# Optimization experiments

Measured on AMD Instinct MI355X. Metric: run time of the kernel, lower is better.

The kernel has to match this reference:

```python
import jax, jax.numpy as jnp
import numpy as np

DIM = 1024      # main_dim
HEADS = 16      # attn_num
HEAD = DIM // HEADS
S = 1024        # seq len per half
BH = 1          # batch per half (x_input batch = 2*BH)
PE = 16; FE = 16      # experts per group
PD = 512; FD = 512    # expert hidden dims
DS = 2048             # shared_expert_dim
K = 4                 # top_k routed experts
EPS = 1e-5
THETA = 10000.0
SCALE_P = 1.0; SCALE_F = 1.0


def rmsnorm(x, w, eps=EPS):
    return x * jax.lax.rsqrt(jnp.mean(x * x, -1, keepdims=True) + eps) * w


def rope(x, theta=THETA):
    # x: [b, h, s, a]; matches RotaryEmb: y1 = x1*cos + x2*sin, y2 = -x1*sin + x2*cos
    a = x.shape[-1]; s = x.shape[2]
    inv = (1.0 / theta) ** (jnp.arange(0, a, 2, dtype=jnp.float32) / a)
    fr = jnp.arange(s, dtype=jnp.float32)[:, None] * inv[None, :]   # [s, a//2]
    cos, sin = jnp.cos(fr), jnp.sin(fr)
    x1, x2 = jnp.split(x, 2, -1)
    return jnp.concatenate([x1 * cos + x2 * sin, -x1 * sin + x2 * cos], -1)


def moe(xt, block, idx, sc):
    # xt: [T, d]; block: [3, E, d, f] (gate/up/down SwiGLU); idx, sc: [T, K]
    g = jnp.einsum('td,edf->tef', xt, block[0])
    u = jnp.einsum('td,edf->tef', xt, block[1])
    h = jax.nn.silu(g) * u
    out_all = jnp.einsum('tef,edf->ted', h, block[2])        # per-expert outputs
    sel = jnp.take_along_axis(out_all, idx[:, :, None], 1)   # [T, K, d]
    return jnp.sum(sel * sc[:, :, None], 1)


def setup_inputs():
    key = jax.random.key(0)
    ks = jax.random.split(key, 16)
    w = 0.02  # param scale for numerical sanity
    d = {}
    d['x_input'] = jax.random.normal(ks[0], (2 * BH, S, DIM), jnp.float32)
    d['p_indices'] = jax.random.randint(ks[1], (BH * S, K), 0, PE)
    d['p_values'] = jax.random.normal(ks[2], (BH * S, K), jnp.float32)
    d['f_indices'] = jax.random.randint(ks[3], (BH * S, K), 0, FE)
    d['f_values'] = jax.random.normal(ks[4], (BH * S, K), jnp.float32)
    d['attn_norm_w'] = jnp.ones((DIM,), jnp.float32)
    d['ffn_norm_w'] = jnp.ones((DIM,), jnp.float32)
    d['W_attn'] = jax.random.normal(ks[5], (DIM, 3 * DIM), jnp.float32) * w
    d['W_attn_o'] = jax.random.normal(ks[6], (DIM, DIM), jnp.float32) * w
    d['ffn_up_w'] = jax.random.normal(ks[7], (DIM, 2 * DS), jnp.float32) * w
    d['ffn_down_w'] = jax.random.normal(ks[8], (DS, DIM), jnp.float32) * w
    d['p_ffn_experts'] = jax.random.normal(ks[9], (3, PE, DIM, PD), jnp.float32) * w
    d['f_ffn_experts'] = jax.random.normal(ks[10], (3, FE, DIM, FD), jnp.float32) * w
    d['p_token_keys'] = jax.random.normal(ks[11], (DIM, PE), jnp.float32) * w
    d['f_token_keys'] = jax.random.normal(ks[12], (DIM, FE), jnp.float32) * w
    d['p_router_bias'] = jnp.zeros((PE,), jnp.float32)
    d['f_router_bias'] = jnp.zeros((FE,), jnp.float32)
    return d


def reference(x_input, p_indices, p_values, f_indices, f_values,
              attn_norm_w, ffn_norm_w, W_attn, W_attn_o, ffn_up_w, ffn_down_w,
              p_ffn_experts, f_ffn_experts, p_token_keys, f_token_keys,
              p_router_bias, f_router_bias):
    B2, s, dim = x_input.shape
    b = B2 // 2
    # attention block
    x = rmsnorm(x_input, attn_norm_w)
    xq, xk, xv = jnp.split(x @ W_attn, 3, -1)
    heads = lambda t: t.reshape(B2, s, HEADS, HEAD).transpose(0, 2, 1, 3)
    xq, xk, xv = heads(xq), heads(xk), heads(xv)
    xq, xk = rope(xq), rope(xk)
    # dual interleave: '(c b) h s a -> b h (s c) a', c=2
    il = lambda t: t.reshape(2, b, HEADS, s, HEAD).transpose(1, 2, 3, 0, 4).reshape(b, HEADS, 2 * s, HEAD)
    q, k, v = il(xq), il(xk), il(xv)
    scores = jnp.einsum('bhqa,bhka->bhqk', q, k) / jnp.sqrt(jnp.float32(HEAD))
    causal = jnp.tril(jnp.ones((2 * s, 2 * s), bool))
    attn = jax.nn.softmax(jnp.where(causal, scores, -jnp.inf), -1)
    o = jnp.einsum('bhqk,bhka->bhqa', attn, v)
    # de-interleave: 'b h (s c) a -> (c b) s (h a)'
    o = o.reshape(b, HEADS, s, 2, HEAD).transpose(3, 0, 2, 1, 4).reshape(B2, s, dim)
    x_ffn_input = o @ W_attn_o + x_input
    x_ffn = rmsnorm(x_ffn_input, ffn_norm_w)
    p_x = x_ffn[:b].reshape(-1, dim)
    f_x = x_ffn[b:].reshape(-1, dim)
    # router: token keys + bias, sigmoid, normalize
    p_vals = p_values + jnp.take_along_axis(p_x @ p_token_keys, p_indices, -1) + p_router_bias[p_indices]
    f_vals = f_values + jnp.take_along_axis(f_x @ f_token_keys, f_indices, -1) + f_router_bias[f_indices]
    p_sc = jax.nn.sigmoid(p_vals)
    p_sc = p_sc / jnp.sum(p_sc, -1, keepdims=True) * SCALE_P
    f_sc = jax.nn.sigmoid(f_vals)
    f_sc = f_sc / jnp.sum(f_sc, -1, keepdims=True) * SCALE_F
    py = moe(p_x, p_ffn_experts, p_indices, p_sc).reshape(b, s, dim)
    fy = moe(f_x, f_ffn_experts, f_indices, f_sc).reshape(b, s, dim)
    y = jnp.concatenate([py, fy], 0) + x_ffn_input
    # shared expert (SwiGLU)
    x1, x2 = jnp.split(x_ffn @ ffn_up_w, 2, -1)
    y = y + (jax.nn.silu(x1) * x2) @ ffn_down_w
    return y
```

## Files before the change

### kernel.cpp

```cpp
#include <hip/hip_runtime.h>


#define T_TOT   2048
#define DMODEL  1024
#define NHEADS  16
#define NEXP    16
#define FDIM    512
#define DSH     2048
#define NPAIR   8192

typedef __attribute__((ext_vector_type(4))) float          f32x4;
typedef __attribute__((ext_vector_type(8))) short          s16x8;
typedef __attribute__((ext_vector_type(8))) unsigned short u16x8;
typedef __attribute__((ext_vector_type(2))) unsigned int   u32x2;

__device__ __forceinline__ float sigm(float x) { return 1.0f / (1.0f + __expf(-x)); }

__device__ __forceinline__ unsigned short bf16r(float f) {
    union { float f; unsigned int u; } v; v.f = f;
    unsigned int r = v.u + 0x7fffu + ((v.u >> 16) & 1u);
    return (unsigned short)(r >> 16);
}

__device__ __forceinline__ unsigned int cvtpk(float lo, float hi) {
    unsigned int r;
    asm("v_cvt_pk_bf16_f32 %0, %1, %2" : "=v"(r) : "v"(lo), "v"(hi));
    return r;
}

__device__ __forceinline__ float ubf(unsigned short u) {
    union { unsigned int i; float f; } v; v.i = (unsigned int)u << 16; return v.f;
}

__device__ __forceinline__ int pair2tok(int p) {
    return ((p >> 12) << 10) + ((p & 4095) >> 2);
}

__global__ void rmsnorm_kernel(const float* __restrict__ x,
                               const float* __restrict__ w,
                               unsigned short* __restrict__ out) {
    int t = blockIdx.x, tid = threadIdx.x;
    float4 xv = *(const float4*)(x + (size_t)t * DMODEL + tid * 4);
    __shared__ float rb[256];
    rb[tid] = xv.x*xv.x + xv.y*xv.y + xv.z*xv.z + xv.w*xv.w;
    __syncthreads();
    for (int s = 128; s > 0; s >>= 1) { if (tid < s) rb[tid] += rb[tid+s]; __syncthreads(); }
    float scale = rsqrtf(rb[0] * (1.0f/1024.0f) + 1e-5f);
    float4 wv = *(const float4*)(w + tid * 4);
    u32x2 pv;
    pv.x = cvtpk(xv.x * scale * wv.x, xv.y * scale * wv.y);
    pv.y = cvtpk(xv.z * scale * wv.z, xv.w * scale * wv.w);
    *(u32x2*)(out + (size_t)t * DMODEL + tid * 4) = pv;
}

__global__ void rope_kernel(unsigned short* __restrict__ qkv) {
    int t = blockIdx.x, tid = threadIdx.x;
    int s = t & 1023;
    unsigned short* row = qkv + (size_t)t * 3072;
    for (int pp = tid; pp < 512; pp += 256) {
        int h = pp >> 5, i = pp & 31;
        float fr = (float)s * exp2f(-0.41524101186092028f * (float)i);
        float sn, cs;
        sincosf(fr, &sn, &cs);
        int o1 = (h << 6) + i, o2 = o1 + 32;
        float x1 = ubf(row[o1]), x2 = ubf(row[o2]);
        row[o1] = bf16r(x1 * cs + x2 * sn);
        row[o2] = bf16r(x2 * cs - x1 * sn);
        x1 = ubf(row[1024 + o1]); x2 = ubf(row[1024 + o2]);
        row[1024 + o1] = bf16r(x1 * cs + x2 * sn);
        row[1024 + o2] = bf16r(x2 * cs - x1 * sn);
    }
}

__global__ __launch_bounds__(256) void attn_mfma_kernel(
        const unsigned short* __restrict__ qkv,
        unsigned short* __restrict__ attn_out) {
    int qt = blockIdx.x, h = blockIdx.y;
    __shared__ alignas(16) unsigned short Qs[64][72];
    __shared__ alignas(16) unsigned short Ks[64][72];
    __shared__ alignas(16) unsigned short Vt[64][72];
    __shared__ alignas(16) unsigned short Ps[4][16][72];
    int tid = threadIdx.x;
    int w = tid >> 6, lane = tid & 63;
    int lr = lane & 15, lkg = lane >> 4, lk = lkg << 3;
    int kr = tid >> 3, kc = (tid & 7) << 3;

    #pragma unroll
    for (int i = 0; i < 2; ++i) {
        int rr = kr + 32 * i;
        int p = qt * 64 + rr;
        int t = ((p & 1) << 10) + (p >> 1);
        u16x8 q = *(const u16x8*)(qkv + (size_t)t * 3072 + (h << 6) + kc);
        unsigned int* dst = (unsigned int*)&Qs[rr][kc];
        dst[0] = cvtpk(ubf(q[0]) * 0.125f, ubf(q[1]) * 0.125f);
        dst[1] = cvtpk(ubf(q[2]) * 0.125f, ubf(q[3]) * 0.125f);
        dst[2] = cvtpk(ubf(q[4]) * 0.125f, ubf(q[5]) * 0.125f);
        dst[3] = cvtpk(ubf(q[6]) * 0.125f, ubf(q[7]) * 0.125f);
    }
    u16x8 pkv[2], pvv[2];
    #pragma unroll
    for (int i = 0; i < 2; ++i) {
        int rr = kr + 32 * i;
        int t = ((rr & 1) << 10) + (rr >> 1);
        const unsigned short* b = qkv + (size_t)t * 3072 + (h << 6) + kc;
        pkv[i] = *(const u16x8*)(b + 1024);
        pvv[i] = *(const u16x8*)(b + 2048);
    }
    __syncthreads();
    s16x8 qa0 = *(const s16x8*)&Qs[(w << 4) + lr][lk];
    s16x8 qa1 = *(const s16x8*)&Qs[(w << 4) + lr][32 + lk];

    float m[4], l[4];
    f32x4 oacc[4];
    #pragma unroll
    for (int r = 0; r < 4; ++r) { m[r] = -1e30f; l[r] = 0.0f; }
    #pragma unroll
    for (int df = 0; df < 4; ++df) oacc[df] = (f32x4)0.0f;

    int qrow_base = qt * 64 + w * 16 + lkg * 4;

    for (int kb = 0; kb <= qt; ++kb) {
        __syncthreads();
        u16x8 ck[2], cv[2];
        #pragma unroll
        for (int i = 0; i < 2; ++i) { ck[i] = pkv[i]; cv[i] = pvv[i]; }
        if (kb + 1 <= qt) {
            #pragma unroll
            for (int i = 0; i < 2; ++i) {
                int rr = kr + 32 * i;
                int p = (kb + 1) * 64 + rr;
                int t = ((p & 1) << 10) + (p >> 1);
                const unsigned short* b = qkv + (size_t)t * 3072 + (h << 6) + kc;
                pkv[i] = *(const u16x8*)(b + 1024);
                pvv[i] = *(const u16x8*)(b + 2048);
            }
        }
        #pragma unroll
        for (int i = 0; i < 2; ++i) {
            int rr = kr + 32 * i;
            *(u16x8*)&Ks[rr][kc] = ck[i];
            #pragma unroll
            for (int j = 0; j < 8; ++j) {
                int vrow = kc + j;
                int sw = ((vrow >> 3) & 7) << 3;
                Vt[vrow][rr ^ sw] = cv[i][j];
            }
        }
        __syncthreads();

        f32x4 s[4];
        #pragma unroll
        for (int nf = 0; nf < 4; ++nf) {
            s16x8 b0 = *(const s16x8*)&Ks[nf * 16 + lr][lk];
            s16x8 b1 = *(const s16x8*)&Ks[nf * 16 + lr][32 + lk];
            f32x4 z = (f32x4)0.0f;
            z = __builtin_amdgcn_mfma_f32_16x16x32_bf16(qa0, b0, z, 0, 0, 0);
            z = __builtin_amdgcn_mfma_f32_16x16x32_bf16(qa1, b1, z, 0, 0, 0);
            s[nf] = z;
        }
        if (kb == qt) {
            #pragma unroll
            for (int nf = 0; nf < 4; ++nf) {
                int kcol = kb * 64 + nf * 16 + lr;
                #pragma unroll
                for (int r = 0; r < 4; ++r)
                    if (kcol > qrow_base + r) s[nf][r] = -1e30f;
            }
        }
        float mloc[4];
        #pragma unroll
        for (int r = 0; r < 4; ++r)
            mloc[r] = fmaxf(fmaxf(s[0][r], s[1][r]), fmaxf(s[2][r], s[3][r]));
        #pragma unroll
        for (int r = 0; r < 4; ++r) {
            mloc[r] = fmaxf(mloc[r], __shfl_xor(mloc[r], 1));
            mloc[r] = fmaxf(mloc[r], __shfl_xor(mloc[r], 2));
            mloc[r] = fmaxf(mloc[r], __shfl_xor(mloc[r], 4));
            mloc[r] = fmaxf(mloc[r], __shfl_xor(mloc[r], 8));
        }
        float alpha[4], psum[4];
        #pragma unroll
        for (int r = 0; r < 4; ++r) {
            float mnew = fmaxf(m[r], mloc[r]);
            alpha[r] = __expf(m[r] - mnew);
            m[r] = mnew;
            psum[r] = 0.0f;
        }
        #pragma unroll
        for (int nf = 0; nf < 4; ++nf)
            #pragma unroll
            for (int r = 0; r < 4; ++r) {
                float pv2 = __expf(s[nf][r] - m[r]);
                s[nf][r] = pv2;
                psum[r] += pv2;
            }
        #pragma unroll
        for (int r = 0; r < 4; ++r) {
            psum[r] += __shfl_xor(psum[r], 1);
            psum[r] += __shfl_xor(psum[r], 2);
            psum[r] += __shfl_xor(psum[r], 4);
            psum[r] += __shfl_xor(psum[r], 8);
            l[r] = l[r] * alpha[r] + psum[r];
        }
        #pragma unroll
        for (int nf = 0; nf < 4; ++nf)
            #pragma unroll
            for (int r = 0; r < 4; ++r)
                Ps[w][lkg * 4 + r][nf * 16 + lr] = bf16r(s[nf][r]);
        #pragma unroll
        for (int df = 0; df < 4; ++df)
            #pragma unroll
            for (int r = 0; r < 4; ++r)
                oacc[df][r] *= alpha[r];
        s16x8 pa0 = *(const s16x8*)&Ps[w][lr][lk];
        s16x8 pa1 = *(const s16x8*)&Ps[w][lr][32 + lk];
        #pragma unroll
        for (int df = 0; df < 4; ++df) {
            int vr = df * 16 + lr;
            int sw = ((vr >> 3) & 7) << 3;
            s16x8 v0 = *(const s16x8*)&Vt[vr][lk ^ sw];
            s16x8 v1 = *(const s16x8*)&Vt[vr][(32 + lk) ^ sw];
            oacc[df] = __builtin_amdgcn_mfma_f32_16x16x32_bf16(pa0, v0, oacc[df], 0, 0, 0);
            oacc[df] = __builtin_amdgcn_mfma_f32_16x16x32_bf16(pa1, v1, oacc[df], 0, 0, 0);
        }
    }

    float invl[4];
    #pragma unroll
    for (int r = 0; r < 4; ++r) invl[r] = 1.0f / l[r];
    #pragma unroll
    for (int r = 0; r < 4; ++r) {
        int qrow = qrow_base + r;
        int t = ((qrow & 1) << 10) + (qrow >> 1);
        unsigned short* op = attn_out + (size_t)t * 1024 + (h << 6) + lr;
        #pragma unroll
        for (int df = 0; df < 4; ++df)
            op[df * 16] = bf16r(oacc[df][r] * invl[r]);
    }
}

__global__ void router_kernel(const unsigned short* __restrict__ xffn,
        const float* __restrict__ p_keys, const float* __restrict__ f_keys,
        const int* __restrict__ p_idx, const int* __restrict__ f_idx,
        const float* __restrict__ p_val, const float* __restrict__ f_val,
        const float* __restrict__ p_bias, const float* __restrict__ f_bias,
        float* __restrict__ sc) {
    int tl = blockIdx.x, hf = blockIdx.y;
    int t = hf * 1024 + tl;
    const float* keys = hf ? f_keys : p_keys;
    const int* idx    = hf ? f_idx  : p_idx;
    const float* val  = hf ? f_val  : p_val;
    const float* bias = hf ? f_bias : p_bias;
    int tid = threadIdx.x;
    float acc[16];
    #pragma unroll
    for (int e = 0; e < 16; ++e) acc[e] = 0.0f;
    const unsigned short* x = xffn + (size_t)t * DMODEL;
    for (int d = tid; d < 1024; d += 256) {
        float xd = ubf(x[d]);
        const float* kr = keys + d * 16;
        #pragma unroll
        for (int e4 = 0; e4 < 4; ++e4) {
            float4 kv = *(const float4*)(kr + e4 * 4);
            acc[e4*4+0] += xd * kv.x;
            acc[e4*4+1] += xd * kv.y;
            acc[e4*4+2] += xd * kv.z;
            acc[e4*4+3] += xd * kv.w;
        }
    }
    #pragma unroll
    for (int e = 0; e < 16; ++e) {
        float v = acc[e];
        v += __shfl_down(v, 32); v += __shfl_down(v, 16); v += __shfl_down(v, 8);
        v += __shfl_down(v, 4);  v += __shfl_down(v, 2);  v += __shfl_down(v, 1);
        acc[e] = v;
    }
    __shared__ float part[4][16];
    __shared__ float logit[16];
    __shared__ float sg[4];
    int wave = tid >> 6, ln = tid & 63;
    if (ln == 0) {
        #pragma unroll
        for (int e = 0; e < 16; ++e) part[wave][e] = acc[e];
    }
    __syncthreads();
    if (tid < 16) logit[tid] = part[0][tid] + part[1][tid] + part[2][tid] + part[3][tid];
    __syncthreads();
    if (tid < 4) {
        int ii = idx[tl * 4 + tid];
        float v = val[tl * 4 + tid] + logit[ii] + bias[ii];
        sg[tid] = 1.0f / (1.0f + expf(-v));
    }
    __syncthreads();
    if (tid < 4) {
        float ssum = sg[0] + sg[1] + sg[2] + sg[3];
        sc[t * 4 + tid] = sg[tid] / ssum;
    }
}

__global__ __launch_bounds__(1024) void buckets_kernel(
        const int* __restrict__ p_idx, const int* __restrict__ f_idx,
        int* __restrict__ counts, int* __restrict__ offsets,
        int* __restrict__ pair_p) {
    __shared__ int lcnt[32], loff[32], lcur[32];
    int tid = threadIdx.x;
    if (tid < 32) { lcnt[tid] = 0; lcur[tid] = 0; }
    __syncthreads();
    for (int p = tid; p < NPAIR; p += 1024) {
        int hf = p >> 12, rem = p & 4095;
        int e = (hf ? f_idx : p_idx)[rem];
        atomicAdd(&lcnt[(hf << 4) + e], 1);
    }
    __syncthreads();
    if (tid == 0) {
        int o = 0;
        for (int b = 0; b < 32; ++b) { loff[b] = o; o += lcnt[b]; }
    }
    __syncthreads();
    for (int p = tid; p < NPAIR; p += 1024) {
        int hf = p >> 12, rem = p & 4095;
        int e = (hf ? f_idx : p_idx)[rem];
        int b = (hf << 4) + e;
        int pos = atomicAdd(&lcur[b], 1);
        pair_p[loff[b] + pos] = p;
    }
    if (tid < 32) { counts[tid] = lcnt[tid]; offsets[tid] = loff[tid]; }
}

template<int MODE, int BN2, int OUTBF>
__global__ __launch_bounds__(256) void mfma_gemm(
        const unsigned short* __restrict__ A, const float* __restrict__ B,
        void* __restrict__ Cv, const float* __restrict__ resid,
        int M, int N, int K) {
    constexpr int NI = BN2 / 32;
    __shared__ alignas(16) unsigned short As[128][40];
    __shared__ alignas(16) unsigned short Bs[BN2][40];
    int tid = threadIdx.x;
    int m0 = blockIdx.y * 128, n0 = blockIdx.x * BN2;
    int w = tid >> 6, lane = tid & 63;
    int wm = (w >> 1) * 64, wn = (w & 1) * (BN2 / 2);
    int lr = lane & 15, lk = (lane >> 4) << 3;
    int ar = tid >> 2, ac = (tid & 3) << 3;
    int bn = (tid >> 3) << 2, bk = (tid & 7) << 2;
    bool bact = true;
    if (BN2 == 64) bact = (tid < 128);
    const unsigned short* Ap0 = A + (size_t)(m0 + ar) * K + ac;
    const unsigned short* Ap1 = Ap0 + (size_t)64 * K;
    const float* Bp = B + (size_t)bk * N + n0 + bn;

    f32x4 acc[4][NI] = {};
    u16x8 a0c, a1c, a0n, a1n;
    f32x4 b_c[4], b_n[4];
    a0c = *(const u16x8*)Ap0;
    a1c = *(const u16x8*)Ap1;
    if (bact) {
        #pragma unroll
        for (int j = 0; j < 4; ++j)
            b_c[j] = *(const f32x4*)(Bp + (size_t)j * N);
    }
    for (int k0 = 0; k0 < K; k0 += 32) {
        __syncthreads();
        if (k0 + 32 < K) {
            a0n = *(const u16x8*)(Ap0 + k0 + 32);
            a1n = *(const u16x8*)(Ap1 + k0 + 32);
            if (bact) {
                const float* bp = Bp + (size_t)(k0 + 32) * N;
                #pragma unroll
                for (int j = 0; j < 4; ++j)
                    b_n[j] = *(const f32x4*)(bp + (size_t)j * N);
            }
        }
        *(u16x8*)&As[ar][ac] = a0c;
        *(u16x8*)&As[ar + 64][ac] = a1c;
        if (bact) {
            #pragma unroll
            for (int jj = 0; jj < 4; ++jj) {
                u32x2 pv;
                pv.x = cvtpk(b_c[0][jj], b_c[1][jj]);
                pv.y = cvtpk(b_c[2][jj], b_c[3][jj]);
                *(u32x2*)&Bs[bn + jj][bk] = pv;
            }
        }
        __syncthreads();
        s16x8 af[4], bfr[NI];
        #pragma unroll
        for (int mi = 0; mi < 4; ++mi)
            af[mi] = *(const s16x8*)&As[wm + mi * 16 + lr][lk];
        #pragma unroll
        for (int ni = 0; ni < NI; ++ni)
            bfr[ni] = *(const s16x8*)&Bs[wn + ni * 16 + lr][lk];
        #pragma unroll
        for (int mi = 0; mi < 4; ++mi)
            #pragma unroll
            for (int ni = 0; ni < NI; ++ni)
                acc[mi][ni] = __builtin_amdgcn_mfma_f32_16x16x32_bf16(
                                  af[mi], bfr[ni], acc[mi][ni], 0, 0, 0);
        a0c = a0n; a1c = a1n;
        #pragma unroll
        for (int j = 0; j < 4; ++j) b_c[j] = b_n[j];
    }
    #pragma unroll
    for (int mi = 0; mi < 4; ++mi)
        #pragma unroll
        for (int r = 0; r < 4; ++r) {
            int row = m0 + wm + mi * 16 + ((lane >> 4) << 2) + r;
            size_t rb = (size_t)row * N + n0 + wn + lr;
            #pragma unroll
            for (int ni = 0; ni < NI; ++ni) {
                size_t off = rb + ni * 16;
                float v = acc[mi][ni][r];
                if constexpr (OUTBF) {
                    ((unsigned short*)Cv)[off] = bf16r(v);
                } else {
                    float* Cf = (float*)Cv;
                    if (MODE == 1) v += Cf[off];
                    if (MODE == 2) v += resid[off];
                    Cf[off] = v;
                }
            }
        }
}

template<int MOE>
__global__ __launch_bounds__(256) void mfma_gateup(
        const unsigned short* __restrict__ X, const float* __restrict__ Wp,
        const float* __restrict__ Wf, const int* __restrict__ pair_p,
        const int* __restrict__ counts, const int* __restrict__ offsets,
        unsigned short* __restrict__ Hout) {
    __shared__ alignas(16) unsigned short As[128][40];
    __shared__ alignas(16) unsigned short Bsg[64][40];
    __shared__ alignas(16) unsigned short Bsu[64][40];
    __shared__ int toks[128];
    int tid = threadIdx.x;
    int rem = 128, slot0 = 0, m0 = 0, n0, ldb;
    const float *Wg, *Wu;
    if (MOE) {
        int bucket = blockIdx.y;
        int cnt = counts[bucket];
        int tile0 = blockIdx.x * 128;
        if (tile0 >= cnt) return;
        n0 = blockIdx.z * 64;
        int e = bucket & 15;
        const float* base = (bucket >> 4) ? Wf : Wp;
        Wg = base + (size_t)e * (DMODEL * FDIM) + n0;
        Wu = base + (size_t)(NEXP + e) * (DMODEL * FDIM) + n0;
        ldb = FDIM;
        slot0 = offsets[bucket] + tile0;
        rem = cnt - tile0;
        if (tid < 128)
            toks[tid] = (tid < rem) ? pair2tok(pair_p[slot0 + tid]) : 0;
    } else {
        m0 = blockIdx.y * 128;
        n0 = blockIdx.x * 64;
        Wg = Wp + n0;
        Wu = Wp + DSH + n0;
        ldb = 2 * DSH;
    }
    int w = tid >> 6, lane = tid & 63;
    int wm = (w >> 1) * 64, wn = (w & 1) * 32;
    int lr = lane & 15, lk = (lane >> 4) << 3;
    int ar = tid >> 2, ac = (tid & 3) << 3;
    int t2 = tid & 127, wq = tid >> 7;
    int bn = (t2 >> 3) << 2, bk = (t2 & 7) << 2;
    const float* bsrc = wq ? Wu : Wg;
    if (MOE) __syncthreads();
    const unsigned short *Xp0, *Xp1;
    {
        int x0 = MOE ? toks[ar] : (m0 + ar);
        int x1 = MOE ? toks[ar + 64] : (m0 + ar + 64);
        Xp0 = X + (size_t)x0 * DMODEL + ac;
        Xp1 = X + (size_t)x1 * DMODEL + ac;
    }
    f32x4 ag[4][2] = {}, au[4][2] = {};
    u16x8 a0c, a1c, a0n, a1n;
    f32x4 b_c[4], b_n[4];
    a0c = *(const u16x8*)Xp0;
    a1c = *(const u16x8*)Xp1;
    const float* Bp = bsrc + (size_t)bk * ldb + bn;
    #pragma unroll
    for (int j = 0; j < 4; ++j)
        b_c[j] = *(const f32x4*)(Bp + (size_t)j * ldb);
    for (int k0 = 0; k0 < DMODEL; k0 += 32) {
        __syncthreads();
        if (k0 + 32 < DMODEL) {
            a0n = *(const u16x8*)(Xp0 + k0 + 32);
            a1n = *(const u16x8*)(Xp1 + k0 + 32);
            const float* bp = Bp + (size_t)(k0 + 32) * ldb;
            #pragma unroll
            for (int j = 0; j < 4; ++j)
                b_n[j] = *(const f32x4*)(bp + (size_t)j * ldb);
        }
        *(u16x8*)&As[ar][ac] = a0c;
        *(u16x8*)&As[ar + 64][ac] = a1c;
        {
            unsigned short (*bl)[40] = wq ? Bsu : Bsg;
            #pragma unroll
            for (int jj = 0; jj < 4; ++jj) {
                u32x2 pv;
                pv.x = cvtpk(b_c[0][jj], b_c[1][jj]);
                pv.y = cvtpk(b_c[2][jj], b_c[3][jj]);
                *(u32x2*)&bl[bn + jj][bk] = pv;
            }
        }
        __syncthreads();
        s16x8 af[4], bg[2], bu[2];
        #pragma unroll
        for (int mi = 0; mi < 4; ++mi)
            af[mi] = *(const s16x8*)&As[wm + mi * 16 + lr][lk];
        #pragma unroll
        for (int ni = 0; ni < 2; ++ni) {
            bg[ni] = *(const s16x8*)&Bsg[wn + ni * 16 + lr][lk];
            bu[ni] = *(const s16x8*)&Bsu[wn + ni * 16 + lr][lk];
        }
        #pragma unroll
        for (int mi = 0; mi < 4; ++mi)
            #pragma unroll
            for (int ni = 0; ni < 2; ++ni) {
                ag[mi][ni] = __builtin_amdgcn_mfma_f32_16x16x32_bf16(
                                 af[mi], bg[ni], ag[mi][ni], 0, 0, 0);
                au[mi][ni] = __builtin_amdgcn_mfma_f32_16x16x32_bf16(
                                 af[mi], bu[ni], au[mi][ni], 0, 0, 0);
            }
        a0c = a0n; a1c = a1n;
        #pragma unroll
        for (int j = 0; j < 4; ++j) b_c[j] = b_n[j];
    }
    #pragma unroll
    for (int mi = 0; mi < 4; ++mi)
        #pragma unroll
        for (int r = 0; r < 4; ++r) {
            int rloc = wm + mi * 16 + ((lane >> 4) << 2) + r;
            if (MOE && rloc >= rem) continue;
            size_t rowb = MOE ? (size_t)(slot0 + rloc) * FDIM
                              : (size_t)(m0 + rloc) * DSH;
            #pragma unroll
            for (int ni = 0; ni < 2; ++ni) {
                float g = ag[mi][ni][r], u = au[mi][ni][r];
                Hout[rowb + n0 + wn + ni * 16 + lr] = bf16r(g * sigm(g) * u);
            }
        }
}

__global__ __launch_bounds__(256) void mfma_moe_down(
        const unsigned short* __restrict__ h_pairs,
        const float* __restrict__ p_experts, const float* __restrict__ f_experts,
        const int* __restrict__ pair_p, const int* __restrict__ counts,
        const int* __restrict__ offsets, const float* __restrict__ sc,
        float* __restrict__ y) {
    __shared__ alignas(16) unsigned short As[128][40];
    __shared__ alignas(16) unsigned short Bs[128][40];
    __shared__ int   tokd[128];
    __shared__ float scd[128];
    int tid = threadIdx.x;
    int bucket = blockIdx.y;
    int cnt = counts[bucket];
    int tile0 = blockIdx.x * 128;
    if (tile0 >= cnt) return;
    int d0 = blockIdx.z * 128;
    int e = bucket & 15;
    const float* base = (bucket >> 4) ? f_experts : p_experts;
    const float* Wd = base + (size_t)(2 * NEXP + e) * (DMODEL * FDIM);
    int slot0 = offsets[bucket] + tile0;
    int rem = cnt - tile0;
    if (tid < 128) {
        int ok = tid < rem;
        int pr = ok ? pair_p[slot0 + tid] : 0;
        tokd[tid] = pair2tok(pr);
        scd[tid]  = ok ? sc[pr] : 0.0f;
    }
    int w = tid >> 6, lane = tid & 63;
    int wm = (w >> 1) * 64, wn = (w & 1) * 64;
    int lr = lane & 15, lk = (lane >> 4) << 3;
    int ar = tid >> 2, ac = (tid & 3) << 3;
    int br = tid >> 3, bc = (tid & 7) << 2;
    const unsigned short* Ap0 = h_pairs + (size_t)(slot0 + ar) * FDIM + ac;
    const unsigned short* Ap1 = Ap0 + (size_t)64 * FDIM;
    const float* Bp0 = Wd + (size_t)(d0 + br) * FDIM + bc;
    f32x4 acc[4][4] = {};
    u16x8 a0c, a1c, a0n, a1n;
    f32x4 b_c[4], b_n[4];
    a0c = *(const u16x8*)Ap0;
    a1c = *(const u16x8*)Ap1;
    #pragma unroll
    for (int i = 0; i < 4; ++i)
        b_c[i] = *(const f32x4*)(Bp0 + (size_t)(32 * i) * FDIM);
    for (int k0 = 0; k0 < FDIM; k0 += 32) {
        __syncthreads();
        if (k0 + 32 < FDIM) {
            a0n = *(const u16x8*)(Ap0 + k0 + 32);
            a1n = *(const u16x8*)(Ap1 + k0 + 32);
            #pragma unroll
            for (int i = 0; i < 4; ++i)
                b_n[i] = *(const f32x4*)(Bp0 + (size_t)(32 * i) * FDIM + k0 + 32);
        }
        *(u16x8*)&As[ar][ac] = a0c;
        *(u16x8*)&As[ar + 64][ac] = a1c;
        #pragma unroll
        for (int i = 0; i < 4; ++i) {
            u32x2 pv;
            pv.x = cvtpk(b_c[i][0], b_c[i][1]);
            pv.y = cvtpk(b_c[i][2], b_c[i][3]);
            *(u32x2*)&Bs[br + 32 * i][bc] = pv;
        }
        __syncthreads();
        s16x8 af[4], bfr[4];
        #pragma unroll
        for (int mi = 0; mi < 4; ++mi)
            af[mi] = *(const s16x8*)&As[wm + mi * 16 + lr][lk];
        #pragma unroll
        for (int ni = 0; ni < 4; ++ni)
            bfr[ni] = *(const s16x8*)&Bs[wn + ni * 16 + lr][lk];
        #pragma unroll
        for (int mi = 0; mi < 4; ++mi)
            #pragma unroll
            for (int ni = 0; ni < 4; ++ni)
                acc[mi][ni] = __builtin_amdgcn_mfma_f32_16x16x32_bf16(
                                  af[mi], bfr[ni], acc[mi][ni], 0, 0, 0);
        a0c = a0n; a1c = a1n;
        #pragma unroll
        for (int i = 0; i < 4; ++i) b_c[i] = b_n[i];
    }
    #pragma unroll
    for (int mi = 0; mi < 4; ++mi)
        #pragma unroll
        for (int r = 0; r < 4; ++r) {
            int rloc = wm + mi * 16 + ((lane >> 4) << 2) + r;
            if (rloc < rem) {
                int   t = tokd[rloc];
                float s = scd[rloc];
                float* yp = y + (size_t)t * DMODEL + d0 + wn + lr;
                #pragma unroll
                for (int ni = 0; ni < 4; ++ni)
                    atomicAdd(yp + ni * 16, s * acc[mi][ni][r]);
            }
        }
}

extern "C" void kernel_launch(void* const* d_in, const int* in_sizes, int n_in,
                              void* d_out, int out_size, void* d_ws, size_t ws_size,
                              hipStream_t stream) {
    const float* x_input  = (const float*)d_in[0];
    const int*   p_idx    = (const int*)d_in[1];
    const float* p_val    = (const float*)d_in[2];
    const int*   f_idx    = (const int*)d_in[3];
    const float* f_val    = (const float*)d_in[4];
    const float* attn_w   = (const float*)d_in[5];
    const float* ffn_w    = (const float*)d_in[6];
    const float* W_attn   = (const float*)d_in[7];
    const float* W_attn_o = (const float*)d_in[8];
    const float* ffn_up   = (const float*)d_in[9];
    const float* ffn_down = (const float*)d_in[10];
    const float* p_exp    = (const float*)d_in[11];
    const float* f_exp    = (const float*)d_in[12];
    const float* p_keys   = (const float*)d_in[13];
    const float* f_keys   = (const float*)d_in[14];
    const float* p_bias   = (const float*)d_in[15];
    const float* f_bias   = (const float*)d_in[16];
    float* y32 = (float*)d_out;
    (void)in_sizes; (void)n_in; (void)out_size; (void)ws_size;

    float* ws = (float*)d_ws;
    unsigned short* xnormh    = (unsigned short*)ws;
    unsigned short* attn_outh = (unsigned short*)ws;
    unsigned short* qkvh      = (unsigned short*)(ws + 2097152);
    unsigned short* h_pairsh  = (unsigned short*)(ws + 2097152);
    unsigned short* hsh       = (unsigned short*)(ws + 2097152);
    float* x_ffn_in  = ws + 8388608;
    unsigned short* x_ffnh = (unsigned short*)(ws + 10485760);
    float* sc        = ws + 12582912;
    int*   counts    = (int*)(ws + 12591104);
    int*   offsets   = counts + 32;
    int*   pair_p    = offsets + 32;

    rmsnorm_kernel<<<T_TOT, 256, 0, stream>>>(x_input, attn_w, xnormh);
    mfma_gemm<0, 128, 1><<<dim3(24, 16), 256, 0, stream>>>(xnormh, W_attn, qkvh,
                                                           nullptr, T_TOT, 3072, 1024);
    rope_kernel<<<T_TOT, 256, 0, stream>>>(qkvh);
    attn_mfma_kernel<<<dim3(32, NHEADS), 256, 0, stream>>>(qkvh, attn_outh);
    mfma_gemm<2, 64, 0><<<dim3(16, 16), 256, 0, stream>>>(attn_outh, W_attn_o,
                                                          x_ffn_in, x_input,
                                                          T_TOT, 1024, 1024);
    rmsnorm_kernel<<<T_TOT, 256, 0, stream>>>(x_ffn_in, ffn_w, x_ffnh);
    router_kernel<<<dim3(1024, 2), 256, 0, stream>>>(x_ffnh, p_keys, f_keys,
                                                     p_idx, f_idx, p_val, f_val,
                                                     p_bias, f_bias, sc);
    buckets_kernel<<<1, 1024, 0, stream>>>(p_idx, f_idx, counts, offsets, pair_p);
    mfma_gateup<1><<<dim3(4, 32, 8), 256, 0, stream>>>(x_ffnh, p_exp, f_exp,
                                                       pair_p, counts, offsets,
                                                       h_pairsh);
    hipMemcpyAsync(y32, x_ffn_in, (size_t)T_TOT * DMODEL * sizeof(float),
                   hipMemcpyDeviceToDevice, stream);
    mfma_moe_down<<<dim3(4, 32, 8), 256, 0, stream>>>(h_pairsh, p_exp, f_exp,
                                                      pair_p, counts, offsets,
                                                      sc, y32);
    mfma_gateup<0><<<dim3(32, 16), 256, 0, stream>>>(x_ffnh, ffn_up, nullptr,
                                                     nullptr, nullptr, nullptr, hsh);
    mfma_gemm<1, 64, 0><<<dim3(16, 16), 256, 0, stream>>>(hsh, ffn_down, y32,
                                                          nullptr, T_TOT, 1024, 2048);
}
```

Baseline: 688.0 us.

## Double-buffer LDS tiles in GEMM, gate-up and down kernels

Converts the three MFMA GEMM kernels from a single LDS tile with two barriers per k-step to ping-pong LDS buffers. Each k-step now computes on one buffer while the other is filled, which removes one barrier per 32-wide k-slice and lets global loads and the bf16 conversion overlap MFMA work. In exchange it doubles LDS use per block, which may lower occupancy, and adds register pressure from a second set of prefetch registers.

```diff
diff --git a/kernel.cpp b/kernel.cpp
--- a/kernel.cpp
+++ b/kernel.cpp
@@ -34,6 +34,49 @@
 
 __device__ __forceinline__ int pair2tok(int p) {
     return ((p >> 12) << 10) + ((p & 4095) >> 2);
+}
+
+template<int NI>
+__device__ __forceinline__ void tile_mma(
+        const unsigned short (*Asb)[40], const unsigned short (*Bsb)[40],
+        int wm, int wn, int lr, int lk, f32x4 (&acc)[4][NI]) {
+    s16x8 af[4], bfr[NI];
+    #pragma unroll
+    for (int mi = 0; mi < 4; ++mi)
+        af[mi] = *(const s16x8*)&Asb[wm + mi * 16 + lr][lk];
+    #pragma unroll
+    for (int ni = 0; ni < NI; ++ni)
+        bfr[ni] = *(const s16x8*)&Bsb[wn + ni * 16 + lr][lk];
+    #pragma unroll
+    for (int mi = 0; mi < 4; ++mi)
+        #pragma unroll
+        for (int ni = 0; ni < NI; ++ni)
+            acc[mi][ni] = __builtin_amdgcn_mfma_f32_16x16x32_bf16(
+                              af[mi], bfr[ni], acc[mi][ni], 0, 0, 0);
+}
+
+__device__ __forceinline__ void gu_mma(
+        const unsigned short (*Asb)[40], const unsigned short (*Bg)[40],
+        const unsigned short (*Bu)[40], int wm, int wn, int lr, int lk,
+        f32x4 (&ag)[4][2], f32x4 (&au)[4][2]) {
+    s16x8 af[4], bg[2], bu[2];
+    #pragma unroll
+    for (int mi = 0; mi < 4; ++mi)
+        af[mi] = *(const s16x8*)&Asb[wm + mi * 16 + lr][lk];
+    #pragma unroll
+    for (int ni = 0; ni < 2; ++ni) {
+        bg[ni] = *(const s16x8*)&Bg[wn + ni * 16 + lr][lk];
+        bu[ni] = *(const s16x8*)&Bu[wn + ni * 16 + lr][lk];
+    }
+    #pragma unroll
+    for (int mi = 0; mi < 4; ++mi)
+        #pragma unroll
+        for (int ni = 0; ni < 2; ++ni) {
+            ag[mi][ni] = __builtin_amdgcn_mfma_f32_16x16x32_bf16(
+                             af[mi], bg[ni], ag[mi][ni], 0, 0, 0);
+            au[mi][ni] = __builtin_amdgcn_mfma_f32_16x16x32_bf16(
+                             af[mi], bu[ni], au[mi][ni], 0, 0, 0);
+        }
 }
 
 __global__ void rmsnorm_kernel(const float* __restrict__ x,
@@ -333,8 +376,8 @@
         void* __restrict__ Cv, const float* __restrict__ resid,
         int M, int N, int K) {
     constexpr int NI = BN2 / 32;
-    __shared__ alignas(16) unsigned short As[128][40];
-    __shared__ alignas(16) unsigned short Bs[BN2][40];
+    __shared__ alignas(16) unsigned short As[2][128][40];
+    __shared__ alignas(16) unsigned short Bs[2][BN2][40];
     int tid = threadIdx.x;
     int m0 = blockIdx.y * 128, n0 = blockIdx.x * BN2;
     int w = tid >> 6, lane = tid & 63;
@@ -349,56 +392,51 @@
     const float* Bp = B + (size_t)bk * N + n0 + bn;
 
     f32x4 acc[4][NI] = {};
-    u16x8 a0c, a1c, a0n, a1n;
-    f32x4 b_c[4], b_n[4];
-    a0c = *(const u16x8*)Ap0;
-    a1c = *(const u16x8*)Ap1;
-    if (bact) {
-        #pragma unroll
-        for (int j = 0; j < 4; ++j)
-            b_c[j] = *(const f32x4*)(Bp + (size_t)j * N);
-    }
-    for (int k0 = 0; k0 < K; k0 += 32) {
+    u16x8 aA0, aA1, aB0, aB1;
+    f32x4 bA[4], bB[4];
+
+#define GM_LOAD(A0, A1, BV, KK) do {                                      \
+        A0 = *(const u16x8*)(Ap0 + (KK));                                 \
+        A1 = *(const u16x8*)(Ap1 + (KK));                                 \
+        if (bact) {                                                       \
+            const float* bp_ = Bp + (size_t)(KK) * N;                     \
+            _Pragma("unroll")                                             \
+            for (int j = 0; j < 4; ++j)                                   \
+                BV[j] = *(const f32x4*)(bp_ + (size_t)j * N);             \
+        }                                                                 \
+    } while (0)
+
+#define GM_WRITE(BUF, A0, A1, BV) do {                                    \
+        *(u16x8*)&As[BUF][ar][ac] = A0;                                   \
+        *(u16x8*)&As[BUF][ar + 64][ac] = A1;                              \
+        if (bact) {                                                       \
+            _Pragma("unroll")                                             \
+            for (int jj = 0; jj < 4; ++jj) {                              \
+                u32x2 pv_;                                                \
+                pv_.x = cvtpk(BV[0][jj], BV[1][jj]);                      \
+                pv_.y = cvtpk(BV[2][jj], BV[3][jj]);                      \
+                *(u32x2*)&Bs[BUF][bn + jj][bk] = pv_;                     \
+            }                                                             \
+        }                                                                 \
+    } while (0)
+
+    GM_LOAD(aA0, aA1, bA, 0);
+    GM_LOAD(aB0, aB1, bB, 32);
+    GM_WRITE(0, aA0, aA1, bA);
+    __syncthreads();
+    for (int k0 = 0; k0 < K; k0 += 64) {
+        if (k0 + 64 < K) GM_LOAD(aA0, aA1, bA, k0 + 64);
+        tile_mma<NI>(As[0], Bs[0], wm, wn, lr, lk, acc);
+        GM_WRITE(1, aB0, aB1, bB);
         __syncthreads();
-        if (k0 + 32 < K) {
-            a0n = *(const u16x8*)(Ap0 + k0 + 32);
-            a1n = *(const u16x8*)(Ap1 + k0 + 32);
-            if (bact) {
-                const float* bp = Bp + (size_t)(k0 + 32) * N;
-                #pragma unroll
-                for (int j = 0; j < 4; ++j)
-                    b_n[j] = *(const f32x4*)(bp + (size_t)j * N);
-            }
-        }
-        *(u16x8*)&As[ar][ac] = a0c;
-        *(u16x8*)&As[ar + 64][ac] = a1c;
-        if (bact) {
-            #pragma unroll
-            for (int jj = 0; jj < 4; ++jj) {
-                u32x2 pv;
-                pv.x = cvtpk(b_c[0][jj], b_c[1][jj]);
-                pv.y = cvtpk(b_c[2][jj], b_c[3][jj]);
-                *(u32x2*)&Bs[bn + jj][bk] = pv;
-            }
-        }
+        if (k0 + 96 < K) GM_LOAD(aB0, aB1, bB, k0 + 96);
+        tile_mma<NI>(As[1], Bs[1], wm, wn, lr, lk, acc);
+        if (k0 + 64 < K) GM_WRITE(0, aA0, aA1, bA);
         __syncthreads();
-        s16x8 af[4], bfr[NI];
-        #pragma unroll
-        for (int mi = 0; mi < 4; ++mi)
-            af[mi] = *(const s16x8*)&As[wm + mi * 16 + lr][lk];
-        #pragma unroll
-        for (int ni = 0; ni < NI; ++ni)
-            bfr[ni] = *(const s16x8*)&Bs[wn + ni * 16 + lr][lk];
-        #pragma unroll
-        for (int mi = 0; mi < 4; ++mi)
-            #pragma unroll
-            for (int ni = 0; ni < NI; ++ni)
-                acc[mi][ni] = __builtin_amdgcn_mfma_f32_16x16x32_bf16(
-                                  af[mi], bfr[ni], acc[mi][ni], 0, 0, 0);
-        a0c = a0n; a1c = a1n;
-        #pragma unroll
-        for (int j = 0; j < 4; ++j) b_c[j] = b_n[j];
-    }
+    }
+#undef GM_LOAD
+#undef GM_WRITE
+
     #pragma unroll
     for (int mi = 0; mi < 4; ++mi)
         #pragma unroll
@@ -427,9 +465,9 @@
         const float* __restrict__ Wf, const int* __restrict__ pair_p,
         const int* __restrict__ counts, const int* __restrict__ offsets,
         unsigned short* __restrict__ Hout) {
-    __shared__ alignas(16) unsigned short As[128][40];
-    __shared__ alignas(16) unsigned short Bsg[64][40];
-    __shared__ alignas(16) unsigned short Bsu[64][40];
+    __shared__ alignas(16) unsigned short As[2][128][40];
+    __shared__ alignas(16) unsigned short Bsg[2][64][40];
+    __shared__ alignas(16) unsigned short Bsu[2][64][40];
     __shared__ int toks[128];
     int tid = threadIdx.x;
     int rem = 128, slot0 = 0, m0 = 0, n0, ldb;
@@ -471,60 +509,54 @@
         Xp0 = X + (size_t)x0 * DMODEL + ac;
         Xp1 = X + (size_t)x1 * DMODEL + ac;
     }
+    const float* Bp = bsrc + (size_t)bk * ldb + bn;
     f32x4 ag[4][2] = {}, au[4][2] = {};
-    u16x8 a0c, a1c, a0n, a1n;
-    f32x4 b_c[4], b_n[4];
-    a0c = *(const u16x8*)Xp0;
-    a1c = *(const u16x8*)Xp1;
-    const float* Bp = bsrc + (size_t)bk * ldb + bn;
-    #pragma unroll
-    for (int j = 0; j < 4; ++j)
-        b_c[j] = *(const f32x4*)(Bp + (size_t)j * ldb);
-    for (int k0 = 0; k0 < DMODEL; k0 += 32) {
+    u16x8 aA0, aA1, aB0, aB1;
+    f32x4 bA[4], bB[4];
+
+#define GU_LOAD(A0, A1, BV, KK) do {                                      \
+        A0 = *(const u16x8*)(Xp0 + (KK));                                 \
+        A1 = *(const u16x8*)(Xp1 + (KK));                                 \
+        {                                                                 \
+            const float* bp_ = Bp + (size_t)(KK) * ldb;                   \
+            _Pragma("unroll")                                             \
+            for (int j = 0; j < 4; ++j)                                   \
+                BV[j] = *(const f32x4*)(bp_ + (size_t)j * ldb);           \
+        }                                                                 \
+    } while (0)
+
+#define GU_WRITE(BUF, A0, A1, BV) do {                                    \
+        *(u16x8*)&As[BUF][ar][ac] = A0;                                   \
+        *(u16x8*)&As[BUF][ar + 64][ac] = A1;                              \
+        {                                                                 \
+            unsigned short (*bl_)[40] = wq ? Bsu[BUF] : Bsg[BUF];         \
+            _Pragma("unroll")                                             \
+            for (int jj = 0; jj < 4; ++jj) {                              \
+                u32x2 pv_;                                                \
+                pv_.x = cvtpk(BV[0][jj], BV[1][jj]);                      \
+                pv_.y = cvtpk(BV[2][jj], BV[3][jj]);                      \
+                *(u32x2*)&bl_[bn + jj][bk] = pv_;                         \
+            }                                                             \
+        }                                                                 \
+    } while (0)
+
+    GU_LOAD(aA0, aA1, bA, 0);
+    GU_LOAD(aB0, aB1, bB, 32);
+    GU_WRITE(0, aA0, aA1, bA);
+    __syncthreads();
+    for (int k0 = 0; k0 < DMODEL; k0 += 64) {
+        if (k0 + 64 < DMODEL) GU_LOAD(aA0, aA1, bA, k0 + 64);
+        gu_mma(As[0], Bsg[0], Bsu[0], wm, wn, lr, lk, ag, au);
+        GU_WRITE(1, aB0, aB1, bB);
         __syncthreads();
-        if (k0 + 32 < DMODEL) {
-            a0n = *(const u16x8*)(Xp0 + k0 + 32);
-            a1n = *(const u16x8*)(Xp1 + k0 + 32);
-            const float* bp = Bp + (size_t)(k0 + 32) * ldb;
-            #pragma unroll
-            for (int j = 0; j < 4; ++j)
-                b_n[j] = *(const f32x4*)(bp + (size_t)j * ldb);
-        }
-        *(u16x8*)&As[ar][ac] = a0c;
-        *(u16x8*)&As[ar + 64][ac] = a1c;
-        {
-            unsigned short (*bl)[40] = wq ? Bsu : Bsg;
-            #pragma unroll
-            for (int jj = 0; jj < 4; ++jj) {
-                u32x2 pv;
-                pv.x = cvtpk(b_c[0][jj], b_c[1][jj]);
-                pv.y = cvtpk(b_c[2][jj], b_c[3][jj]);
-                *(u32x2*)&bl[bn + jj][bk] = pv;
-            }
-        }
+        if (k0 + 96 < DMODEL) GU_LOAD(aB0, aB1, bB, k0 + 96);
+        gu_mma(As[1], Bsg[1], Bsu[1], wm, wn, lr, lk, ag, au);
+        if (k0 + 64 < DMODEL) GU_WRITE(0, aA0, aA1, bA);
         __syncthreads();
-        s16x8 af[4], bg[2], bu[2];
-        #pragma unroll
-        for (int mi = 0; mi < 4; ++mi)
-            af[mi] = *(const s16x8*)&As[wm + mi * 16 + lr][lk];
-        #pragma unroll
-        for (int ni = 0; ni < 2; ++ni) {
-            bg[ni] = *(const s16x8*)&Bsg[wn + ni * 16 + lr][lk];
-            bu[ni] = *(const s16x8*)&Bsu[wn + ni * 16 + lr][lk];
-        }
-        #pragma unroll
-        for (int mi = 0; mi < 4; ++mi)
-            #pragma unroll
-            for (int ni = 0; ni < 2; ++ni) {
-                ag[mi][ni] = __builtin_amdgcn_mfma_f32_16x16x32_bf16(
-                                 af[mi], bg[ni], ag[mi][ni], 0, 0, 0);
-                au[mi][ni] = __builtin_amdgcn_mfma_f32_16x16x32_bf16(
-                                 af[mi], bu[ni], au[mi][ni], 0, 0, 0);
-            }
-        a0c = a0n; a1c = a1n;
-        #pragma unroll
-        for (int j = 0; j < 4; ++j) b_c[j] = b_n[j];
-    }
+    }
+#undef GU_LOAD
+#undef GU_WRITE
+
     #pragma unroll
     for (int mi = 0; mi < 4; ++mi)
         #pragma unroll
@@ -547,8 +579,8 @@
         const int* __restrict__ pair_p, const int* __restrict__ counts,
         const int* __restrict__ offsets, const float* __restrict__ sc,
         float* __restrict__ y) {
-    __shared__ alignas(16) unsigned short As[128][40];
-    __shared__ alignas(16) unsigned short Bs[128][40];
+    __shared__ alignas(16) unsigned short As[2][128][40];
+    __shared__ alignas(16) unsigned short Bs[2][128][40];
     __shared__ int   tokd[128];
     __shared__ float scd[128];
     int tid = threadIdx.x;
@@ -577,49 +609,46 @@
     const unsigned short* Ap1 = Ap0 + (size_t)64 * FDIM;
     const float* Bp0 = Wd + (size_t)(d0 + br) * FDIM + bc;
     f32x4 acc[4][4] = {};
-    u16x8 a0c, a1c, a0n, a1n;
-    f32x4 b_c[4], b_n[4];
-    a0c = *(const u16x8*)Ap0;
-    a1c = *(const u16x8*)Ap1;
-    #pragma unroll
-    for (int i = 0; i < 4; ++i)
-        b_c[i] = *(const f32x4*)(Bp0 + (size_t)(32 * i) * FDIM);
-    for (int k0 = 0; k0 < FDIM; k0 += 32) {
+    u16x8 aA0, aA1, aB0, aB1;
+    f32x4 bA[4], bB[4];
+
+#define MD_LOAD(A0, A1, BV, KK) do {                                      \
+        A0 = *(const u16x8*)(Ap0 + (KK));                                 \
+        A1 = *(const u16x8*)(Ap1 + (KK));                                 \
+        _Pragma("unroll")                                                 \
+        for (int i = 0; i < 4; ++i)                                       \
+            BV[i] = *(const f32x4*)(Bp0 + (size_t)(32 * i) * FDIM + (KK));\
+    } while (0)
+
+#define MD_WRITE(BUF, A0, A1, BV) do {                                    \
+        *(u16x8*)&As[BUF][ar][ac] = A0;                                   \
+        *(u16x8*)&As[BUF][ar + 64][ac] = A1;                              \
+        _Pragma("unroll")                                                 \
+        for (int i = 0; i < 4; ++i) {                                     \
+            u32x2 pv_;                                                    \
+            pv_.x = cvtpk(BV[i][0], BV[i][1]);                            \
+            pv_.y = cvtpk(BV[i][2], BV[i][3]);                            \
+            *(u32x2*)&Bs[BUF][br + 32 * i][bc] = pv_;                     \
+        }                                                                 \
+    } while (0)
+
+    MD_LOAD(aA0, aA1, bA, 0);
+    MD_LOAD(aB0, aB1, bB, 32);
+    MD_WRITE(0, aA0, aA1, bA);
+    __syncthreads();
+    for (int k0 = 0; k0 < FDIM; k0 += 64) {
+        if (k0 + 64 < FDIM) MD_LOAD(aA0, aA1, bA, k0 + 64);
+        tile_mma<4>(As[0], Bs[0], wm, wn, lr, lk, acc);
+        MD_WRITE(1, aB0, aB1, bB);
         __syncthreads();
-        if (k0 + 32 < FDIM) {
-            a0n = *(const u16x8*)(Ap0 + k0 + 32);
-            a1n = *(const u16x8*)(Ap1 + k0 + 32);
-            #pragma unroll
-            for (int i = 0; i < 4; ++i)
-                b_n[i] = *(const f32x4*)(Bp0 + (size_t)(32 * i) * FDIM + k0 + 32);
-        }
-        *(u16x8*)&As[ar][ac] = a0c;
-        *(u16x8*)&As[ar + 64][ac] = a1c;
-        #pragma unroll
-        for (int i = 0; i < 4; ++i) {
-            u32x2 pv;
-            pv.x = cvtpk(b_c[i][0], b_c[i][1]);
-            pv.y = cvtpk(b_c[i][2], b_c[i][3]);
-            *(u32x2*)&Bs[br + 32 * i][bc] = pv;
-        }
+        if (k0 + 96 < FDIM) MD_LOAD(aB0, aB1, bB, k0 + 96);
+        tile_mma<4>(As[1], Bs[1], wm, wn, lr, lk, acc);
+        if (k0 + 64 < FDIM) MD_WRITE(0, aA0, aA1, bA);
         __syncthreads();
-        s16x8 af[4], bfr[4];
-        #pragma unroll
-        for (int mi = 0; mi < 4; ++mi)
-            af[mi] = *(const s16x8*)&As[wm + mi * 16 + lr][lk];
-        #pragma unroll
-        for (int ni = 0; ni < 4; ++ni)
-            bfr[ni] = *(const s16x8*)&Bs[wn + ni * 16 + lr][lk];
-        #pragma unroll
-        for (int mi = 0; mi < 4; ++mi)
-            #pragma unroll
-            for (int ni = 0; ni < 4; ++ni)
-                acc[mi][ni] = __builtin_amdgcn_mfma_f32_16x16x32_bf16(
-                                  af[mi], bfr[ni], acc[mi][ni], 0, 0, 0);
-        a0c = a0n; a1c = a1n;
-        #pragma unroll
-        for (int i = 0; i < 4; ++i) b_c[i] = b_n[i];
-    }
+    }
+#undef MD_LOAD
+#undef MD_WRITE
+
     #pragma unroll
     for (int mi = 0; mi < 4; ++mi)
         #pragma unroll
```

Result: faster. 628.2 us (-8.7%).
